# Performance work log

Measured on AMD Instinct MI355X. Metric: run time of the kernel, lower is better.

## Reference

```python
import jax, jax.numpy as jnp
import numpy as np

N_NODES = 100000


def setup_inputs() -> dict:
    key = jax.random.key(0)
    k1, k2, k3 = jax.random.split(key, 3)
    feat = jax.random.normal(k1, (N_NODES, 64), dtype=jnp.float32)
    src = jax.random.randint(k2, (1250000,), 0, N_NODES, dtype=jnp.int64)
    dst = jax.random.randint(k3, (1250000,), 0, N_NODES, dtype=jnp.int64)
    return {"feat": feat, "src": src, "dst": dst}


def reference(feat, src, dst):
    # GraphConv(norm='both', activation=None): degree-normalized neighbor sum
    # with implicit self-connection (rst = feat_dst + sum_neighbors), where
    # degrees are clamp(min=1) + 1 to account for the self edge.
    n = feat.shape[0]
    ones = jnp.ones(src.shape[0], dtype=feat.dtype)
    out_deg = jax.ops.segment_sum(ones, src, num_segments=n)
    in_deg = jax.ops.segment_sum(ones, dst, num_segments=n)
    norm_l = jax.lax.rsqrt(jnp.maximum(out_deg, 1.0) + 1.0)  # [N]
    norm_r = jax.lax.rsqrt(jnp.maximum(in_deg, 1.0) + 1.0)   # [N]
    feat_src = feat * norm_l[:, None]                         # left-normalize
    msgs = feat_src[src]                                      # gather [E, D]
    h_neigh = jax.ops.segment_sum(msgs, dst, num_segments=n)  # scatter-sum [N, D]
    rst = (feat + h_neigh) * norm_r[:, None]                  # right-normalize
    return rst
```

## Files before the change

### kernel.cpp

```cpp
#include <hip/hip_runtime.h>


#define GC_D 64
#define PBITS 8
#define PSIZE 256
#define SCAP 4096
#define EPB 8192
#define MAXPART 512
#define GC_CAP 64


__global__ __launch_bounds__(512) void partition_kernel(
        const int* __restrict__ src,
        const int* __restrict__ dst,
        int* __restrict__ curA,
        int* __restrict__ curB,
        int* __restrict__ streamA,
        unsigned char* __restrict__ streamB,
        int e, int nPart) {
    __shared__ int histA[MAXPART], histB[MAXPART], baseA[MAXPART], baseB[MAXPART];
    __shared__ int lcurA[MAXPART], lcurB[MAXPART];
    int t = threadIdx.x;
    for (int i = t; i < nPart; i += 512) {
        histA[i] = 0; histB[i] = 0; lcurA[i] = 0; lcurB[i] = 0;
    }
    __syncthreads();
    int lo = blockIdx.x * EPB;
    int hi = min(lo + EPB, e);
    for (int i = lo + t; i < hi; i += 512) {
        int s = src[i], d = dst[i];
        atomicAdd(&histA[d >> PBITS], 1);
        atomicAdd(&histB[s >> PBITS], 1);
    }
    __syncthreads();
    for (int i = t; i < nPart; i += 512) {
        int hA = histA[i];
        baseA[i] = hA ? atomicAdd(&curA[i], hA) : 0;
        int hB = histB[i];
        baseB[i] = hB ? atomicAdd(&curB[i], hB) : 0;
    }
    __syncthreads();
    for (int i = lo + t; i < hi; i += 512) {
        int s = src[i], d = dst[i];
        int pA = d >> PBITS;
        int posA = baseA[pA] + atomicAdd(&lcurA[pA], 1);
        if (posA < SCAP) streamA[pA * SCAP + posA] = s | ((d & 255) << 17);
        int pB = s >> PBITS;
        int posB = baseB[pB] + atomicAdd(&lcurB[pB], 1);
        if (posB < SCAP) streamB[pB * SCAP + posB] = (unsigned char)(s & 255);
    }
}

__global__ __launch_bounds__(512) void convertB_kernel(
        const int* __restrict__ curB,
        const unsigned char* __restrict__ streamB,
        const float* __restrict__ feat,
        unsigned short* __restrict__ featb,
        int n) {
    __shared__ int lodeg[PSIZE];
    int p = blockIdx.x, t = threadIdx.x;
    if (t < PSIZE) lodeg[t] = 0;
    __syncthreads();
    int cB = min(curB[p], SCAP);
    const unsigned char* sB = streamB + (size_t)p * SCAP;
    for (int i = t; i < cB; i += 512) atomicAdd(&lodeg[sB[i]], 1);
    __syncthreads();
    int wave = t >> 6, lane = t & 63;
    int g = p * PSIZE;
    for (int r = wave; r < PSIZE; r += 8) {
        int node = g + r;
        if (node >= n) break;
        float nl = rsqrtf(fmaxf((float)lodeg[r], 1.0f) + 1.0f);
        float v = feat[(size_t)node * GC_D + lane] * nl;
        unsigned bb = __float_as_uint(v);
        bb = (bb + 0x7FFFu + ((bb >> 16) & 1u)) >> 16;
        featb[(size_t)node * GC_D + lane] = (unsigned short)bb;
    }
    if (p == 0 && t < GC_D) featb[(size_t)n * GC_D + t] = 0;
}

__global__ __launch_bounds__(1024) void sortgather_kernel(
        const int* __restrict__ curA,
        const int* __restrict__ streamA,
        const float* __restrict__ feat,
        const unsigned short* __restrict__ featb,
        float* __restrict__ out,
        int n) {
    __shared__ int sAl[SCAP];
    __shared__ int lperm[SCAP];
    __shared__ int lcnt[PSIZE], loff[PSIZE], lcur[PSIZE];
    int p = blockIdx.x, t = threadIdx.x;
    if (t < PSIZE) lcnt[t] = 0;
    __syncthreads();
    int cA = min(curA[p], SCAP);
    const int* sA = streamA + (size_t)p * SCAP;
    for (int i = t; i < cA; i += 1024) {
        int v = sA[i];
        sAl[i] = v;
        atomicAdd(&lcnt[(v >> 17) & 255], 1);
    }
    __syncthreads();
    if (t < PSIZE) loff[t] = lcnt[t];
    __syncthreads();
    for (int off = 1; off < PSIZE; off <<= 1) {
        int a = (t < PSIZE && t >= off) ? loff[t - off] : 0;
        __syncthreads();
        if (t < PSIZE) loff[t] += a;
        __syncthreads();
    }
    if (t < PSIZE) { loff[t] -= lcnt[t]; lcur[t] = 0; }
    __syncthreads();
    for (int i = t; i < cA; i += 1024) {
        int v = sAl[i];
        int bin = (v >> 17) & 255;
        int pos = loff[bin] + atomicAdd(&lcur[bin], 1);
        lperm[pos] = v & 0x1FFFF;
    }
    __syncthreads();
    int wave = t >> 6, lane = t & 63;
    int half = lane >> 5;
    int c = lane & 31;
    int g = p * PSIZE;
    for (int r = wave; r < PSIZE; r += 16) {
        int node = g + r;
        if (node >= n) break;
        int deg = lcnt[r];
        int off = loff[r];
        float acc0 = 0.0f, acc1 = 0.0f;
        for (int base = 0; base < deg; base += 64) {
            int m = min(deg - base, 64);
            int s_l = (lane < m) ? lperm[off + base + lane] : n;
            int m16 = (m + 15) & ~15;
            for (int j = 0; j < m16; j += 16) {
#pragma unroll
                for (int k = 0; k < 8; ++k) {
                    int s = __shfl(s_l, j + 2 * k + half);
                    unsigned u = *(const unsigned*)(featb + (size_t)s * GC_D + 2 * c);
                    acc0 += __uint_as_float(u << 16);
                    acc1 += __uint_as_float(u & 0xFFFF0000u);
                }
            }
        }
        acc0 += __shfl_xor(acc0, 32);
        acc1 += __shfl_xor(acc1, 32);
        if (half == 0) {
            float nr = rsqrtf(fmaxf((float)deg, 1.0f) + 1.0f);
            const float2 self = *(const float2*)(feat + (size_t)node * GC_D + 2 * c);
            float2 rr;
            rr.x = (self.x + acc0) * nr;
            rr.y = (self.y + acc1) * nr;
            *(float2*)(out + (size_t)node * GC_D + 2 * c) = rr;
        }
    }
}


__global__ void zero_int_kernel(int* __restrict__ p, int n) {
    int i = blockIdx.x * blockDim.x + threadIdx.x;
    if (i < n) p[i] = 0;
}

__global__ void bucket_hist_kernel(const int* __restrict__ src,
                                   const int* __restrict__ dst,
                                   int* __restrict__ cnt,
                                   int* __restrict__ outdeg,
                                   int* __restrict__ bucket,
                                   int e) {
    int i = blockIdx.x * blockDim.x + threadIdx.x;
    if (i < e) {
        int s = src[i];
        int d = dst[i];
        atomicAdd(&outdeg[s], 1);
        int pos = atomicAdd(&cnt[d], 1);
        if (pos < GC_CAP) bucket[d * GC_CAP + pos] = s;
    }
}

__global__ void convert_kernel(const float* __restrict__ feat,
                               const int* __restrict__ outdeg,
                               unsigned short* __restrict__ featb,
                               int n) {
    int i = blockIdx.x * blockDim.x + threadIdx.x;
    int total = (n + 1) * GC_D;
    if (i >= total) return;
    int row = i >> 6;
    if (row >= n) { featb[i] = 0; return; }
    float nl = rsqrtf(fmaxf((float)outdeg[row], 1.0f) + 1.0f);
    unsigned b = __float_as_uint(feat[i] * nl);
    b = (b + 0x7FFFu + ((b >> 16) & 1u)) >> 16;
    featb[i] = (unsigned short)b;
}

__global__ __launch_bounds__(256) void gather_bf16_kernel(
        const float* __restrict__ feat,
        const unsigned short* __restrict__ featb,
        const int* __restrict__ bucket,
        const int* __restrict__ cnt,
        float* __restrict__ out,
        int n) {
    int wid = (blockIdx.x * blockDim.x + threadIdx.x) >> 6;
    int lane = threadIdx.x & 63;
    if (wid >= n) return;
    int deg = cnt[wid];
    int s_raw = bucket[wid * GC_CAP + lane];
    int m = min(deg, GC_CAP);
    int s_l = (lane < m) ? s_raw : n;
    int half = lane >> 5;
    int c = lane & 31;
    float acc0 = 0.0f, acc1 = 0.0f;
    int m16 = (m + 15) & ~15;
    for (int j = 0; j < m16; j += 16) {
#pragma unroll
        for (int k = 0; k < 8; ++k) {
            int s = __shfl(s_l, j + 2 * k + half);
            unsigned u = *(const unsigned*)(featb + (size_t)s * GC_D + 2 * c);
            acc0 += __uint_as_float(u << 16);
            acc1 += __uint_as_float(u & 0xFFFF0000u);
        }
    }
    acc0 += __shfl_xor(acc0, 32);
    acc1 += __shfl_xor(acc1, 32);
    if (half == 0) {
        float nr = rsqrtf(fmaxf((float)deg, 1.0f) + 1.0f);
        const float2 self = *(const float2*)(feat + (size_t)wid * GC_D + 2 * c);
        float2 r;
        r.x = (self.x + acc0) * nr;
        r.y = (self.y + acc1) * nr;
        *(float2*)(out + (size_t)wid * GC_D + 2 * c) = r;
    }
}


extern "C" void kernel_launch(void* const* d_in, const int* in_sizes, int n_in,
                              void* d_out, int out_size, void* d_ws, size_t ws_size,
                              hipStream_t stream) {
    const float* feat = (const float*)d_in[0];
    const int*   src  = (const int*)d_in[1];
    const int*   dst  = (const int*)d_in[2];
    float* out = (float*)d_out;

    const int n = in_sizes[0] / GC_D;
    const int e = in_sizes[1];
    const int nPart = (n + PSIZE - 1) >> PBITS;

    size_t featb_ints = ((size_t)(n + 1) * GC_D + 1) / 2;
    size_t o = 2 * (size_t)nPart;
    o = (o + 31) & ~(size_t)31;
    size_t streamA_o = o;  o += (size_t)nPart * SCAP;
    size_t featb_o = o;    o += featb_ints;
    size_t need_main = o * sizeof(int) + (size_t)nPart * SCAP;

    size_t featb_bytes = (size_t)(n + 1) * GC_D * sizeof(unsigned short);
    size_t need_bf16 = ((size_t)2 * n + (size_t)n * GC_CAP) * sizeof(int) + featb_bytes;

    bool main_ok = (ws_size >= need_main) && nPart <= MAXPART && n <= 131071;

    if (main_ok) {
        int* ws = (int*)d_ws;
        int* curA = ws;
        int* curB = ws + nPart;
        int* streamA = ws + streamA_o;
        unsigned short* featb = (unsigned short*)(ws + featb_o);
        unsigned char* streamB = (unsigned char*)(ws + o);

        hipMemsetAsync(curA, 0, 2 * (size_t)nPart * sizeof(int), stream);
        partition_kernel<<<(e + EPB - 1) / EPB, 512, 0, stream>>>(
            src, dst, curA, curB, streamA, streamB, e, nPart);
        convertB_kernel<<<nPart, 512, 0, stream>>>(curB, streamB, feat, featb, n);
        sortgather_kernel<<<nPart, 1024, 0, stream>>>(curA, streamA, feat, featb,
                                                      out, n);
    } else if (ws_size >= need_bf16) {
        int* cnt    = (int*)d_ws;
        int* outdeg = cnt + n;
        int* bucket = outdeg + n;
        unsigned short* featb = (unsigned short*)(bucket + (size_t)n * GC_CAP);

        zero_int_kernel<<<(2 * n + 255) / 256, 256, 0, stream>>>(cnt, 2 * n);
        bucket_hist_kernel<<<(e + 255) / 256, 256, 0, stream>>>(src, dst, cnt,
                                                                outdeg, bucket, e);
        int totalc = (n + 1) * GC_D;
        convert_kernel<<<(totalc + 255) / 256, 256, 0, stream>>>(feat, outdeg,
                                                                 featb, n);
        long long total = (long long)n * GC_D;
        gather_bf16_kernel<<<(int)((total + 255) / 256), 256, 0, stream>>>(
            feat, featb, bucket, cnt, out, n);
    }
}
```

Measured before the change: 163.5 us.

## Process two destination nodes per wave to overlap gathers; halve partition EPB

The aggregation loop now handles two destination rows per wave at once, issuing both rows' bf16 feature gathers into register arrays before accumulating. This raises memory-level parallelism and hides gather latency, at the cost of more registers and possibly lower occupancy. Rows with more than 64 neighbours fall back to a serial tail loop. Separately, edges-per-block in the partition kernel is halved, which gives more blocks with less work each.

```diff
diff --git a/kernel.cpp b/kernel.cpp
--- a/kernel.cpp
+++ b/kernel.cpp
@@ -5,7 +5,7 @@
 #define PBITS 8
 #define PSIZE 256
 #define SCAP 4096
-#define EPB 8192
+#define EPB 4096
 #define MAXPART 512
 #define GC_CAP 64
 
@@ -121,35 +121,89 @@
     int half = lane >> 5;
     int c = lane & 31;
     int g = p * PSIZE;
-    for (int r = wave; r < PSIZE; r += 16) {
-        int node = g + r;
-        if (node >= n) break;
-        int deg = lcnt[r];
-        int off = loff[r];
-        float acc0 = 0.0f, acc1 = 0.0f;
-        for (int base = 0; base < deg; base += 64) {
-            int m = min(deg - base, 64);
-            int s_l = (lane < m) ? lperm[off + base + lane] : n;
+    for (int rr = wave; rr < PSIZE; rr += 32) {
+        int rA = rr, rB = rr + 16;
+        int nodeA = g + rA, nodeB = g + rB;
+        int degA = lcnt[rA], degB = lcnt[rB];
+        int offA = loff[rA], offB = loff[rB];
+        int mA = min(degA, 64), mB = min(degB, 64);
+        int s_lA = (lane < mA) ? lperm[offA + lane] : n;
+        int s_lB = (lane < mB) ? lperm[offB + lane] : n;
+        float a0 = 0.f, a1 = 0.f, b0 = 0.f, b1 = 0.f;
+        int mA16 = (mA + 15) & ~15, mB16 = (mB + 15) & ~15;
+        int mx = mA16 > mB16 ? mA16 : mB16;
+        for (int j = 0; j < mx; j += 16) {
+            unsigned uA[8], uB[8];
+#pragma unroll
+            for (int k = 0; k < 8; ++k) {
+                int s = __shfl(s_lA, j + 2 * k + half);
+                uA[k] = *(const unsigned*)(featb + (size_t)s * GC_D + 2 * c);
+            }
+#pragma unroll
+            for (int k = 0; k < 8; ++k) {
+                int s = __shfl(s_lB, j + 2 * k + half);
+                uB[k] = *(const unsigned*)(featb + (size_t)s * GC_D + 2 * c);
+            }
+#pragma unroll
+            for (int k = 0; k < 8; ++k) {
+                a0 += __uint_as_float(uA[k] << 16);
+                a1 += __uint_as_float(uA[k] & 0xFFFF0000u);
+            }
+#pragma unroll
+            for (int k = 0; k < 8; ++k) {
+                b0 += __uint_as_float(uB[k] << 16);
+                b1 += __uint_as_float(uB[k] & 0xFFFF0000u);
+            }
+        }
+        for (int base = 64; base < degA; base += 64) {
+            int m = min(degA - base, 64);
+            int s_l = (lane < m) ? lperm[offA + base + lane] : n;
             int m16 = (m + 15) & ~15;
             for (int j = 0; j < m16; j += 16) {
 #pragma unroll
                 for (int k = 0; k < 8; ++k) {
                     int s = __shfl(s_l, j + 2 * k + half);
                     unsigned u = *(const unsigned*)(featb + (size_t)s * GC_D + 2 * c);
-                    acc0 += __uint_as_float(u << 16);
-                    acc1 += __uint_as_float(u & 0xFFFF0000u);
+                    a0 += __uint_as_float(u << 16);
+                    a1 += __uint_as_float(u & 0xFFFF0000u);
                 }
             }
         }
-        acc0 += __shfl_xor(acc0, 32);
-        acc1 += __shfl_xor(acc1, 32);
+        for (int base = 64; base < degB; base += 64) {
+            int m = min(degB - base, 64);
+            int s_l = (lane < m) ? lperm[offB + base + lane] : n;
+            int m16 = (m + 15) & ~15;
+            for (int j = 0; j < m16; j += 16) {
+#pragma unroll
+                for (int k = 0; k < 8; ++k) {
+                    int s = __shfl(s_l, j + 2 * k + half);
+                    unsigned u = *(const unsigned*)(featb + (size_t)s * GC_D + 2 * c);
+                    b0 += __uint_as_float(u << 16);
+                    b1 += __uint_as_float(u & 0xFFFF0000u);
+                }
+            }
+        }
+        a0 += __shfl_xor(a0, 32);
+        a1 += __shfl_xor(a1, 32);
+        b0 += __shfl_xor(b0, 32);
+        b1 += __shfl_xor(b1, 32);
         if (half == 0) {
-            float nr = rsqrtf(fmaxf((float)deg, 1.0f) + 1.0f);
-            const float2 self = *(const float2*)(feat + (size_t)node * GC_D + 2 * c);
-            float2 rr;
-            rr.x = (self.x + acc0) * nr;
-            rr.y = (self.y + acc1) * nr;
-            *(float2*)(out + (size_t)node * GC_D + 2 * c) = rr;
+            if (nodeA < n) {
+                float nr = rsqrtf(fmaxf((float)degA, 1.0f) + 1.0f);
+                const float2 self = *(const float2*)(feat + (size_t)nodeA * GC_D + 2 * c);
+                float2 rv;
+                rv.x = (self.x + a0) * nr;
+                rv.y = (self.y + a1) * nr;
+                *(float2*)(out + (size_t)nodeA * GC_D + 2 * c) = rv;
+            }
+            if (nodeB < n) {
+                float nr = rsqrtf(fmaxf((float)degB, 1.0f) + 1.0f);
+                const float2 self = *(const float2*)(feat + (size_t)nodeB * GC_D + 2 * c);
+                float2 rv;
+                rv.x = (self.x + b0) * nr;
+                rv.y = (self.y + b1) * nr;
+                *(float2*)(out + (size_t)nodeB * GC_D + 2 * c) = rv;
+            }
         }
     }
 }
```

Measured after the change: 174.4 us. 6.6% more time.
